# Kernel optimization log

Hardware: AMD Instinct MI355X
Metric: run time of the kernel (lower is better)

Reference implementation:

```python
import jax, jax.numpy as jnp
import numpy as np

EPS = 1e-6  # clamp for arccosh domain, matching Lorentz-manifold impls


def setup_inputs() -> dict:
    key = jax.random.key(0)
    k1, k2 = jax.random.split(key)
    B, T, D, C = 2, 2048, 256, 32000
    x = jax.random.normal(k1, (B, T, D), dtype=jnp.float32)
    # lt.weight: (num_classes, num_features+1); first column is the time coord
    # which normalize() overwrites, so random init is fine.
    lt_weight = jax.random.normal(k2, (C, D + 1), dtype=jnp.float32) * 0.02
    return {"x": x, "lt_weight": lt_weight}


def reference(x, lt_weight):
    B, T, D = x.shape
    xf = x.reshape(B * T, D)                                  # (N, D) spatial coords
    x0 = jnp.sqrt(1.0 + jnp.sum(xf * xf, axis=1))             # (N,) time coord, lift onto hyperboloid
    # normalize class prototypes onto the hyperboloid: recompute time coord
    cs = lt_weight[:, 1:]                                     # (C, D) spatial
    c0 = jnp.sqrt(1.0 + jnp.sum(cs * cs, axis=1))             # (C,)
    # Minkowski inner product <u,v>_L = -u0*v0 + <u_s, v_s>; distance = arccosh(-<u,v>_L)
    inner = x0[:, None] * c0[None, :] - xf @ cs.T             # (N, C), fused GEMM + rank-1 outer
    dist = jnp.arccosh(jnp.clip(inner, 1.0 + EPS))            # clamp into arccosh domain
    logits = (-dist).reshape(B, T, -1)                        # (B, T, C)
    return logits
```

## Files before the change

kernel.cpp:

```cpp
#include <hip/hip_runtime.h>
#include <hip/hip_bf16.h>


#define M_ROWS   4096
#define N_COLS   32000
#define K_DIM    256
#define LT_LD    257
#define BK       32

typedef __bf16 v8bf __attribute__((ext_vector_type(8)));
typedef float  v4f  __attribute__((ext_vector_type(4)));

#define XB_OFF   0u
#define CB_OFF   2097152u
#define X0_OFF   18481152u
#define C0_OFF   18497536u
#define WS_NEED  18625536u

__global__ __launch_bounds__(256) void prep_kernel(
    const float* __restrict__ x, const float* __restrict__ lt,
    __hip_bfloat16* __restrict__ xb, __hip_bfloat16* __restrict__ cb,
    float* __restrict__ x0, float* __restrict__ c0) {
  int row  = blockIdx.x * 4 + (threadIdx.x >> 6);
  int lane = threadIdx.x & 63;
  if (row >= M_ROWS + N_COLS) return;

  float v[4];
  float ss = 0.0f;
  if (row < M_ROWS) {
    const float* src = x + (size_t)row * K_DIM;
#pragma unroll
    for (int k = 0; k < 4; ++k) { v[k] = src[k * 64 + lane]; ss += v[k] * v[k]; }
  } else {
    int c = row - M_ROWS;
    const float* src = lt + (size_t)c * LT_LD + 1;
#pragma unroll
    for (int k = 0; k < 4; ++k) { v[k] = src[k * 64 + lane]; ss += v[k] * v[k]; }
  }
#pragma unroll
  for (int off = 32; off > 0; off >>= 1) ss += __shfl_down(ss, off, 64);

  __hip_bfloat16* dst = (row < M_ROWS) ? (xb + (size_t)row * K_DIM)
                                       : (cb + (size_t)(row - M_ROWS) * K_DIM);
#pragma unroll
  for (int k = 0; k < 4; ++k) dst[k * 64 + lane] = __float2bfloat16(v[k]);

  if (lane == 0) {
    float n = sqrtf(1.0f + ss);
    if (row < M_ROWS) x0[row] = n; else c0[row - M_ROWS] = n;
  }
}

__device__ __forceinline__ void gload_lds16(const unsigned short* g,
                                            unsigned short* l) {
  __builtin_amdgcn_global_load_lds(
      (const __attribute__((address_space(1))) void*)g,
      (__attribute__((address_space(3))) void*)l,
      16 , 0, 0);
}

__global__ __launch_bounds__(256) void gemm_kernel(
    const unsigned short* __restrict__ xb, const unsigned short* __restrict__ cb,
    const float* __restrict__ x0, const float* __restrict__ c0,
    float* __restrict__ out) {
  __shared__ __attribute__((aligned(16))) unsigned short Al[128 * BK];
  __shared__ __attribute__((aligned(16))) unsigned short Bl[128 * BK];

  const int tid  = threadIdx.x;
  const int w    = tid >> 6;
  const int lane = tid & 63;
  const int wm   = (w >> 1) * 64;
  const int wn   = (w & 1) * 64;
  const int lrow = lane & 15;
  const int lk   = (lane >> 4) * 8;

  const int mbase = blockIdx.y * 128;
  const int nbase = blockIdx.x * 128;

  const unsigned short* gA = xb + (size_t)(mbase + (tid >> 2)) * K_DIM + (tid & 3) * 8;
  const unsigned short* gB = cb + (size_t)(nbase + (tid >> 2)) * K_DIM + (tid & 3) * 8;
  unsigned short* lA = &Al[tid * 8];
  unsigned short* lB = &Bl[tid * 8];
  const size_t rstep = (size_t)64 * K_DIM;

  v4f acc[4][4];
#pragma unroll
  for (int i = 0; i < 4; ++i)
#pragma unroll
    for (int j = 0; j < 4; ++j) acc[i][j] = (v4f){0.f, 0.f, 0.f, 0.f};

#pragma unroll 1
  for (int ki = 0; ki < 8; ++ki) {
    if (ki) __syncthreads();
    const int ko = ki * BK;
    gload_lds16(gA + ko,         lA);
    gload_lds16(gA + rstep + ko, lA + 64 * BK);
    gload_lds16(gB + ko,         lB);
    gload_lds16(gB + rstep + ko, lB + 64 * BK);
    __syncthreads();

    v8bf af[4], bf[4];
#pragma unroll
    for (int i = 0; i < 4; ++i)
      af[i] = *(const v8bf*)(&Al[(wm + i * 16 + lrow) * BK + lk]);
#pragma unroll
    for (int j = 0; j < 4; ++j)
      bf[j] = *(const v8bf*)(&Bl[(wn + j * 16 + lrow) * BK + lk]);
#pragma unroll
    for (int i = 0; i < 4; ++i)
#pragma unroll
      for (int j = 0; j < 4; ++j)
        acc[i][j] = __builtin_amdgcn_mfma_f32_16x16x32_bf16(af[i], bf[j], acc[i][j], 0, 0, 0);
  }

  const int mloc = mbase + wm + (lane >> 4) * 4;
  const int nloc = nbase + wn + lrow;
  float cv[4];
#pragma unroll
  for (int j = 0; j < 4; ++j) cv[j] = c0[nloc + j * 16];

#pragma unroll
  for (int i = 0; i < 4; ++i) {
#pragma unroll
    for (int r = 0; r < 4; ++r) {
      const int m = mloc + i * 16 + r;
      const float xn = x0[m];
#pragma unroll
      for (int j = 0; j < 4; ++j) {
        float inner = xn * cv[j] - acc[i][j][r];
        float vv = fmaxf(inner, 1.000001f);
        float u  = vv + sqrtf(vv * vv - 1.0f);
        __builtin_nontemporal_store(-__logf(u),
                                    &out[(size_t)m * N_COLS + nloc + j * 16]);
      }
    }
  }
}

__global__ __launch_bounds__(256) void naive_kernel(
    const float* __restrict__ x, const float* __restrict__ lt,
    float* __restrict__ out) {
  int n = blockIdx.x * 256 + threadIdx.x;
  int m = blockIdx.y;
  if (n >= N_COLS) return;
  const float* xr = x + (size_t)m * K_DIM;
  const float* cr = lt + (size_t)n * LT_LD + 1;
  float ssx = 0.f, ssc = 0.f, dot = 0.f;
  for (int k = 0; k < K_DIM; ++k) {
    float xv = xr[k], cv = cr[k];
    ssx += xv * xv; ssc += cv * cv; dot += xv * cv;
  }
  float inner = sqrtf(1.f + ssx) * sqrtf(1.f + ssc) - dot;
  float vv = fmaxf(inner, 1.000001f);
  out[(size_t)m * N_COLS + n] = -logf(vv + sqrtf(vv * vv - 1.f));
}

extern "C" void kernel_launch(void* const* d_in, const int* in_sizes, int n_in,
                              void* d_out, int out_size, void* d_ws, size_t ws_size,
                              hipStream_t stream) {
  const float* x  = (const float*)d_in[0];
  const float* lt = (const float*)d_in[1];
  float* out = (float*)d_out;

  if (ws_size >= (size_t)WS_NEED) {
    char* ws = (char*)d_ws;
    __hip_bfloat16* xb = (__hip_bfloat16*)(ws + XB_OFF);
    __hip_bfloat16* cb = (__hip_bfloat16*)(ws + CB_OFF);
    float* x0 = (float*)(ws + X0_OFF);
    float* c0 = (float*)(ws + C0_OFF);

    prep_kernel<<<(M_ROWS + N_COLS) / 4, 256, 0, stream>>>(x, lt, xb, cb, x0, c0);
    gemm_kernel<<<dim3(N_COLS / 128, M_ROWS / 128), 256, 0, stream>>>(
        (const unsigned short*)xb, (const unsigned short*)cb, x0, c0, out);
  } else {
    naive_kernel<<<dim3((N_COLS + 255) / 256, M_ROWS), 256, 0, stream>>>(x, lt, out);
  }
}
```

Measured before the change: 645.3 us.

## Double-buffer LDS tiles, swizzle LDS layout, and remap blocks across XCDs

```diff
diff --git a/kernel.cpp b/kernel.cpp
--- a/kernel.cpp
+++ b/kernel.cpp
@@ -7,6 +7,8 @@
 #define K_DIM    256
 #define LT_LD    257
 #define BK       32
+#define NT_REAL  250
+#define NT_PAD   256
 
 typedef __bf16 v8bf __attribute__((ext_vector_type(8)));
 typedef float  v4f  __attribute__((ext_vector_type(4)));
@@ -59,12 +61,16 @@
       16 , 0, 0);
 }
 
+__device__ __forceinline__ int swz_chunk(int row, int c) {
+  return (row * 4 + ((c ^ row) & 3)) ^ (row & 4);
+}
+
 __global__ __launch_bounds__(256) void gemm_kernel(
     const unsigned short* __restrict__ xb, const unsigned short* __restrict__ cb,
     const float* __restrict__ x0, const float* __restrict__ c0,
     float* __restrict__ out) {
-  __shared__ __attribute__((aligned(16))) unsigned short Al[128 * BK];
-  __shared__ __attribute__((aligned(16))) unsigned short Bl[128 * BK];
+  __shared__ __attribute__((aligned(16))) unsigned short Al[2][128 * BK];
+  __shared__ __attribute__((aligned(16))) unsigned short Bl[2][128 * BK];
 
   const int tid  = threadIdx.x;
   const int w    = tid >> 6;
@@ -72,16 +78,32 @@
   const int wm   = (w >> 1) * 64;
   const int wn   = (w & 1) * 64;
   const int lrow = lane & 15;
-  const int lk   = (lane >> 4) * 8;
-
-  const int mbase = blockIdx.y * 128;
-  const int nbase = blockIdx.x * 128;
-
-  const unsigned short* gA = xb + (size_t)(mbase + (tid >> 2)) * K_DIM + (tid & 3) * 8;
-  const unsigned short* gB = cb + (size_t)(nbase + (tid >> 2)) * K_DIM + (tid & 3) * 8;
-  unsigned short* lA = &Al[tid * 8];
-  unsigned short* lB = &Bl[tid * 8];
-  const size_t rstep = (size_t)64 * K_DIM;
+  const int c16  = lane >> 4;
+
+  const int b   = blockIdx.x;
+  const int xcd = b & 7;
+  const int i5  = b >> 3;
+  const int nt  = (i5 >> 5) * 8 + xcd;
+  const int mt  = i5 & 31;
+  if (nt >= NT_REAL) return;
+  const int mbase = mt * 128;
+  const int nbase = nt * 128;
+
+  const int p0  = tid, p1 = tid + 256;
+  const int rl0 = ((p0 >> 3) << 1) | (((p0 >> 2) ^ (p0 >> 4)) & 1);
+  const int cl0 = (p0 ^ rl0) & 3;
+  const int rl1 = ((p1 >> 3) << 1) | (((p1 >> 2) ^ (p1 >> 4)) & 1);
+  const int cl1 = (p1 ^ rl1) & 3;
+  const unsigned short* gA0 = xb + (size_t)(mbase + rl0) * K_DIM + cl0 * 8;
+  const unsigned short* gA1 = xb + (size_t)(mbase + rl1) * K_DIM + cl1 * 8;
+  const unsigned short* gB0 = cb + (size_t)(nbase + rl0) * K_DIM + cl0 * 8;
+  const unsigned short* gB1 = cb + (size_t)(nbase + rl1) * K_DIM + cl1 * 8;
+
+  int swA[4], swB[4];
+#pragma unroll
+  for (int i = 0; i < 4; ++i) swA[i] = swz_chunk(wm + i * 16 + lrow, c16) * 8;
+#pragma unroll
+  for (int j = 0; j < 4; ++j) swB[j] = swz_chunk(wn + j * 16 + lrow, c16) * 8;
 
   v4f acc[4][4];
 #pragma unroll
@@ -89,28 +111,34 @@
 #pragma unroll
     for (int j = 0; j < 4; ++j) acc[i][j] = (v4f){0.f, 0.f, 0.f, 0.f};
 
-#pragma unroll 1
+  gload_lds16(gA0, &Al[0][tid * 8]);
+  gload_lds16(gA1, &Al[0][(tid + 256) * 8]);
+  gload_lds16(gB0, &Bl[0][tid * 8]);
+  gload_lds16(gB1, &Bl[0][(tid + 256) * 8]);
+  __syncthreads();
+
+#pragma unroll
   for (int ki = 0; ki < 8; ++ki) {
-    if (ki) __syncthreads();
-    const int ko = ki * BK;
-    gload_lds16(gA + ko,         lA);
-    gload_lds16(gA + rstep + ko, lA + 64 * BK);
-    gload_lds16(gB + ko,         lB);
-    gload_lds16(gB + rstep + ko, lB + 64 * BK);
-    __syncthreads();
-
+    const int cur = ki & 1;
+    if (ki < 7) {
+      const int ko = (ki + 1) * BK;
+      const int nb = cur ^ 1;
+      gload_lds16(gA0 + ko, &Al[nb][tid * 8]);
+      gload_lds16(gA1 + ko, &Al[nb][(tid + 256) * 8]);
+      gload_lds16(gB0 + ko, &Bl[nb][tid * 8]);
+      gload_lds16(gB1 + ko, &Bl[nb][(tid + 256) * 8]);
+    }
     v8bf af[4], bf[4];
 #pragma unroll
-    for (int i = 0; i < 4; ++i)
-      af[i] = *(const v8bf*)(&Al[(wm + i * 16 + lrow) * BK + lk]);
-#pragma unroll
-    for (int j = 0; j < 4; ++j)
-      bf[j] = *(const v8bf*)(&Bl[(wn + j * 16 + lrow) * BK + lk]);
+    for (int i = 0; i < 4; ++i) af[i] = *(const v8bf*)(&Al[cur][swA[i]]);
+#pragma unroll
+    for (int j = 0; j < 4; ++j) bf[j] = *(const v8bf*)(&Bl[cur][swB[j]]);
 #pragma unroll
     for (int i = 0; i < 4; ++i)
 #pragma unroll
       for (int j = 0; j < 4; ++j)
         acc[i][j] = __builtin_amdgcn_mfma_f32_16x16x32_bf16(af[i], bf[j], acc[i][j], 0, 0, 0);
+    if (ki < 7) __syncthreads();
   }
 
   const int mloc = mbase + wm + (lane >> 4) * 4;
@@ -170,7 +198,7 @@
     float* c0 = (float*)(ws + C0_OFF);
 
     prep_kernel<<<(M_ROWS + N_COLS) / 4, 256, 0, stream>>>(x, lt, xb, cb, x0, c0);
-    gemm_kernel<<<dim3(N_COLS / 128, M_ROWS / 128), 256, 0, stream>>>(
+    gemm_kernel<<<NT_PAD * 32, 256, 0, stream>>>(
         (const unsigned short*)xb, (const unsigned short*)cb, x0, c0, out);
   } else {
     naive_kernel<<<dim3((N_COLS + 255) / 256, M_ROWS), 256, 0, stream>>>(x, lt, out);
```

New measurement: 606.4 us. 6.0% less time.
